# Kernel tuning notes

Measured on AMD Instinct MI355X. Metric: run time of the kernel, lower is better.

The kernel has to match this reference:

```python
import jax, jax.numpy as jnp
import numpy as np

B, T, C, H = 8, 2048, 1024, 64


def setup_inputs() -> dict:
    key = jax.random.key(0)
    kx, kq, kk, kv = jax.random.split(key, 4)
    sc = 1.0 / np.sqrt(C)
    return {
        "x": jax.random.normal(kx, (B, T, C), dtype=jnp.float32),
        "Wq": jax.random.normal(kq, (C, H), dtype=jnp.float32) * sc,
        "Wk": jax.random.normal(kk, (C, H), dtype=jnp.float32) * sc,
        "Wv": jax.random.normal(kv, (C, H), dtype=jnp.float32) * sc,
    }


def reference(x, Wq, Wk, Wv):
    # Projections: Linear(C, head_size, bias=False) == x @ W
    q = jnp.einsum("btc,ch->bth", x, Wq)
    k = jnp.einsum("btc,ch->bth", x, Wk)
    v = jnp.einsum("btc,ch->bth", x, Wv)
    head_size = q.shape[-1]
    scale = head_size ** -0.5
    # scores: [B, T, T]
    scores = jnp.einsum("bqh,bkh->bqk", q, k) * scale
    # causal mask (tril==0 -> -inf)
    causal = jnp.tril(jnp.ones((scores.shape[1], scores.shape[2]), dtype=bool))
    scores = jnp.where(causal, scores, -jnp.inf)
    w = jax.nn.softmax(scores, axis=-1)
    # dropout_rate=0.0 -> identity
    out = jnp.einsum("bqk,bkh->bqh", w, v)
    return out
```

## Files before the change

kernel.cpp:

```cpp
#include <hip/hip_runtime.h>
#include <hip/hip_bf16.h>
#include <cstdint>
#include <cstddef>

typedef short bf16x8 __attribute__((ext_vector_type(8)));
typedef float f32x4 __attribute__((ext_vector_type(4)));

#define BN 8
#define TN 2048
#define CN 1024
#define HN 64

__device__ __forceinline__ unsigned short f2bf(float f) {
    unsigned int u = __float_as_uint(f);
    u += 0x7fffu + ((u >> 16) & 1u);
    return (unsigned short)(u >> 16);
}

__device__ __forceinline__ int pk2(float lo, float hi) {
    float2 t; t.x = lo; t.y = hi;
    __hip_bfloat162 h = __float22bfloat162_rn(t);
    return *reinterpret_cast<int*>(&h);
}

__device__ __forceinline__ void gload_lds16(const unsigned short* gsrc, void* ldst) {
    __builtin_amdgcn_global_load_lds(
        (const __attribute__((address_space(1))) unsigned int*)gsrc,
        (__attribute__((address_space(3))) unsigned int*)ldst,
        16, 0, 0);
}

__global__ __launch_bounds__(256) void wconv_kernel(const float* __restrict__ Wq,
                                                    const float* __restrict__ Wk,
                                                    const float* __restrict__ Wv,
                                                    unsigned short* __restrict__ Wp) {
    int idx = blockIdx.x * 256 + threadIdx.x;
    int n = idx >> 10;
    int c = idx & 1023;
    int m = n >> 6;
    int h = n & 63;
    const float* W = (m == 0) ? Wq : ((m == 1) ? Wk : Wv);
    float v = W[c * 64 + h];
    if (m == 0) v *= 0.18033688011112042f;
    const int tile = n >> 4, lq = n & 15;
    const int kk = c >> 5, lg = (c >> 3) & 3, e = c & 7;
    Wp[(size_t)(((tile * 32 + kk) * 64 + lg * 16 + lq) * 8 + e)] = f2bf(v);
}

__global__ __launch_bounds__(256) void proj_kernel(const float* __restrict__ X,
                                                   const unsigned short* __restrict__ Wp,
                                                   unsigned short* __restrict__ Qs,
                                                   unsigned short* __restrict__ Kp,
                                                   unsigned short* __restrict__ Vp) {
    __shared__ short Xs[2][32 * 64];
    __shared__ short Wsh[2][6144];

    const int tid = threadIdx.x;
    const int w   = tid >> 6;
    const int l   = tid & 63;
    const int lq  = l & 15;
    const int lg  = l >> 4;
    const int wr   = w >> 1;
    const int nsub = w & 1;
    const int bid = blockIdx.x;
    const int mtile = bid & 511;
    const int nh    = bid >> 9;
    const int rowbase = mtile * 32;

    const int xrow = tid >> 3;
    const int xcol = (tid & 7) * 8;
    const float* xsrc = X + (size_t)(rowbase + xrow) * CN + xcol;
    const int xdst = xrow * 128 + ((xcol * 2) ^ ((xrow & 7) << 4));

    const unsigned short* wsrcc[3];
    int wdstc[3];
    #pragma unroll
    for (int i = 0; i < 3; ++i) {
        const int c = w * 3 + i;
        const int t = c >> 1, kkL = c & 1;
        wsrcc[i] = Wp + (size_t)((nh * 6 + t) * 32 + kkL) * 512 + l * 8;
        wdstc[i] = c * 1024;
    }

    const int arow = wr * 16 + lq;
    int aaddr[2];
    #pragma unroll
    for (int kkL = 0; kkL < 2; ++kkL)
        aaddr[kkL] = arow * 128 + (((kkL * 64 + lg * 16)) ^ ((arow & 7) << 4));
    int baddr[2][3];
    #pragma unroll
    for (int kkL = 0; kkL < 2; ++kkL)
        #pragma unroll
        for (int jj = 0; jj < 3; ++jj) {
            const int t = nsub * 3 + jj;
            baddr[kkL][jj] = ((t * 2 + kkL) * 512 + l * 8) * 2;
        }

    const f32x4 zero4 = {0.f, 0.f, 0.f, 0.f};
    f32x4 acc[3] = {zero4, zero4, zero4};

    {
        #pragma unroll
        for (int i = 0; i < 3; ++i)
            gload_lds16(wsrcc[i], (char*)Wsh[0] + wdstc[i]);
        float4 xa = *(const float4*)(xsrc);
        float4 xb = *(const float4*)(xsrc + 4);
        int4 xc;
        xc.x = pk2(xa.x, xa.y); xc.y = pk2(xa.z, xa.w);
        xc.z = pk2(xb.x, xb.y); xc.w = pk2(xb.z, xb.w);
        *(int4*)((char*)Xs[0] + xdst) = xc;
        __syncthreads();
    }

    for (int s = 0; s < 16; ++s) {
        const int cur = s & 1;
        const int nxt = cur ^ 1;
        const bool more = (s + 1) < 16;
        float4 xa, xb;
        if (more) {
            xa = *(const float4*)(xsrc + (s + 1) * 64);
            xb = *(const float4*)(xsrc + (s + 1) * 64 + 4);
            #pragma unroll
            for (int i = 0; i < 3; ++i)
                gload_lds16(wsrcc[i] + (s + 1) * 1024, (char*)Wsh[nxt] + wdstc[i]);
        }
        #pragma unroll
        for (int kkL = 0; kkL < 2; ++kkL) {
            bf16x8 a  = *(const bf16x8*)((char*)Xs[cur] + aaddr[kkL]);
            bf16x8 b0 = *(const bf16x8*)((char*)Wsh[cur] + baddr[kkL][0]);
            bf16x8 b1 = *(const bf16x8*)((char*)Wsh[cur] + baddr[kkL][1]);
            bf16x8 b2 = *(const bf16x8*)((char*)Wsh[cur] + baddr[kkL][2]);
            acc[0] = __builtin_amdgcn_mfma_f32_16x16x32_bf16(a, b0, acc[0], 0, 0, 0);
            acc[1] = __builtin_amdgcn_mfma_f32_16x16x32_bf16(a, b1, acc[1], 0, 0, 0);
            acc[2] = __builtin_amdgcn_mfma_f32_16x16x32_bf16(a, b2, acc[2], 0, 0, 0);
        }
        if (more) {
            int4 xc;
            xc.x = pk2(xa.x, xa.y); xc.y = pk2(xa.z, xa.w);
            xc.z = pk2(xb.x, xb.y); xc.w = pk2(xb.z, xb.w);
            *(int4*)((char*)Xs[nxt] + xdst) = xc;
        }
        __syncthreads();
    }

    #pragma unroll
    for (int jj = 0; jj < 3; ++jj) {
        const int col = nh * 96 + nsub * 48 + jj * 16 + lq;
        const int mtx = col >> 6;
        const int h   = col & 63;
        #pragma unroll
        for (int i = 0; i < 4; ++i) {
            const int g = rowbase + wr * 16 + 4 * lg + i;
            const unsigned short val = f2bf(acc[jj][i]);
            const int b = g >> 11, tloc = g & 2047;
            const int kt = tloc >> 5;
            if (mtx == 0) {
                Qs[(size_t)g * 64 + h] = val;
            } else if (mtx == 1) {
                const int fa = (tloc >> 4) & 1, lqk = tloc & 15;
                const int ks = h >> 5, lgk = (h >> 3) & 3, e = h & 7;
                Kp[(size_t)(b * 64 + kt) * 2048 + (fa * 2 + ks) * 512 +
                   (lgk * 16 + lqk) * 8 + e] = val;
            } else {
                const int tt = tloc & 31;
                const int lgv = (tt & 15) >> 2;
                const int e = (tt < 16) ? (tt & 3) : 4 + (tt & 3);
                const int nf = h >> 4, lqv = h & 15;
                Vp[(size_t)(b * 64 + kt) * 2048 + nf * 512 +
                   (lgv * 16 + lqv) * 8 + e] = val;
            }
        }
    }
}

__global__ __launch_bounds__(256) void attn_kernel(const unsigned short* __restrict__ Qs,
                                                   const unsigned short* __restrict__ Kp,
                                                   const unsigned short* __restrict__ Vp,
                                                   float* __restrict__ Out) {
    __shared__ float lm[4][16];
    __shared__ float ll[4][16];
    __shared__ float facc[4][1024];

    const int tid = threadIdx.x;
    const int w  = tid >> 6;
    const int l  = tid & 63;
    const int lq = l & 15;
    const int lg = l >> 4;
    const int bid = blockIdx.x;
    const int qt = 127 - (bid >> 3);
    const int b  = bid & 7;
    const int q0 = qt * 16;
    const int nt = (qt >> 1) + 1;

    const unsigned short* Qb = Qs + (size_t)b * TN * 64;
    const unsigned short* KVbase_k = Kp + (size_t)b * 64 * 2048 + (size_t)l * 8;
    const unsigned short* KVbase_v = Vp + (size_t)b * 64 * 2048 + (size_t)l * 8;

    const f32x4 zero4 = {0.f, 0.f, 0.f, 0.f};

    bf16x8 qa0 = *(const bf16x8*)(Qb + (size_t)(q0 + lq) * 64 + lg * 8);
    bf16x8 qa1 = *(const bf16x8*)(Qb + (size_t)(q0 + lq) * 64 + 32 + lg * 8);

    f32x4 acc[4] = {zero4, zero4, zero4, zero4};
    float mrow = -1e30f;
    float lrow = 0.f;

    bf16x8 Kc[4], Vc[4], Kn[4], Vn[4];
    int kt = w;
    if (kt < nt) {
        const size_t tb = (size_t)kt * 2048;
        #pragma unroll
        for (int i = 0; i < 4; ++i) {
            Kc[i] = *(const bf16x8*)(KVbase_k + tb + i * 512);
            Vc[i] = *(const bf16x8*)(KVbase_v + tb + i * 512);
        }
    }

    for (; kt < nt; kt += 4) {
        const int ktn = kt + 4;
        if (ktn < nt) {
            const size_t tb = (size_t)ktn * 2048;
            #pragma unroll
            for (int i = 0; i < 4; ++i) {
                Kn[i] = *(const bf16x8*)(KVbase_k + tb + i * 512);
                Vn[i] = *(const bf16x8*)(KVbase_v + tb + i * 512);
            }
        }

        const int key0 = kt * 32;
        f32x4 s[2];
        s[0] = __builtin_amdgcn_mfma_f32_16x16x32_bf16(Kc[0], qa0, zero4, 0, 0, 0);
        s[0] = __builtin_amdgcn_mfma_f32_16x16x32_bf16(Kc[1], qa1, s[0], 0, 0, 0);
        s[1] = __builtin_amdgcn_mfma_f32_16x16x32_bf16(Kc[2], qa0, zero4, 0, 0, 0);
        s[1] = __builtin_amdgcn_mfma_f32_16x16x32_bf16(Kc[3], qa1, s[1], 0, 0, 0);

        if (kt == nt - 1) {
            const int q = q0 + lq;
            #pragma unroll
            for (int fa = 0; fa < 2; ++fa)
                #pragma unroll
                for (int r = 0; r < 4; ++r) {
                    const int key = key0 + fa * 16 + 4 * lg + r;
                    if (key > q) s[fa][r] = -1e30f;
                }
        }

        float m1 = fmaxf(fmaxf(s[0][0], s[0][1]), s[0][2]);
        float m2 = fmaxf(fmaxf(s[0][3], s[1][0]), s[1][1]);
        float m3 = fmaxf(fmaxf(s[1][2], s[1][3]), m1);
        float tm = fmaxf(m2, m3);
        tm = fmaxf(tm, __shfl_xor(tm, 16));
        tm = fmaxf(tm, __shfl_xor(tm, 32));

        if (!__all(tm <= mrow + 8.0f)) {
            const float mnew = fmaxf(mrow, tm);
            const float cc = __builtin_amdgcn_exp2f(mrow - mnew);
            lrow *= cc;
            float cb[4];
            #pragma unroll
            for (int i = 0; i < 4; ++i) cb[i] = __shfl(cc, 4 * lg + i);
            #pragma unroll
            for (int nf = 0; nf < 4; ++nf)
                #pragma unroll
                for (int i = 0; i < 4; ++i) acc[nf][i] *= cb[i];
            mrow = mnew;
        }

        float p[2][4];
        float psum = 0.f;
        #pragma unroll
        for (int fa = 0; fa < 2; ++fa)
            #pragma unroll
            for (int r = 0; r < 4; ++r) {
                p[fa][r] = __builtin_amdgcn_exp2f(s[fa][r] - mrow);
                psum += p[fa][r];
            }
        psum += __shfl_xor(psum, 16);
        psum += __shfl_xor(psum, 32);
        lrow += psum;

        bf16x8 pa;
        pa[0] = (short)f2bf(p[0][0]); pa[1] = (short)f2bf(p[0][1]);
        pa[2] = (short)f2bf(p[0][2]); pa[3] = (short)f2bf(p[0][3]);
        pa[4] = (short)f2bf(p[1][0]); pa[5] = (short)f2bf(p[1][1]);
        pa[6] = (short)f2bf(p[1][2]); pa[7] = (short)f2bf(p[1][3]);

        acc[0] = __builtin_amdgcn_mfma_f32_16x16x32_bf16(pa, Vc[0], acc[0], 0, 0, 0);
        acc[1] = __builtin_amdgcn_mfma_f32_16x16x32_bf16(pa, Vc[1], acc[1], 0, 0, 0);
        acc[2] = __builtin_amdgcn_mfma_f32_16x16x32_bf16(pa, Vc[2], acc[2], 0, 0, 0);
        acc[3] = __builtin_amdgcn_mfma_f32_16x16x32_bf16(pa, Vc[3], acc[3], 0, 0, 0);

        #pragma unroll
        for (int i = 0; i < 4; ++i) { Kc[i] = Kn[i]; Vc[i] = Vn[i]; }
    }

    if (lg == 0) {
        lm[w][lq] = mrow;
        ll[w][lq] = lrow;
    }
    #pragma unroll
    for (int nf = 0; nf < 4; ++nf)
        #pragma unroll
        for (int i = 0; i < 4; ++i)
            facc[w][(4 * lg + i) * 64 + nf * 16 + lq] = acc[nf][i];

    __syncthreads();

    #pragma unroll
    for (int ii = 0; ii < 4; ++ii) {
        const int e = tid + ii * 256;
        const int q = e >> 6;
        const int h = e & 63;
        const float M = fmaxf(fmaxf(lm[0][q], lm[1][q]),
                              fmaxf(lm[2][q], lm[3][q]));
        float L = 0.f, O = 0.f;
        #pragma unroll
        for (int c = 0; c < 4; ++c) {
            const float wgt = __builtin_amdgcn_exp2f(lm[c][q] - M);
            L += wgt * ll[c][q];
            O += wgt * facc[c][q * 64 + h];
        }
        Out[((size_t)b * TN + q0 + q) * 64 + h] = O / L;
    }
}

extern "C" void kernel_launch(void* const* d_in, const int* in_sizes, int n_in,
                              void* d_out, int out_size, void* d_ws, size_t ws_size,
                              hipStream_t stream) {
    const float* X  = (const float*)d_in[0];
    const float* Wq = (const float*)d_in[1];
    const float* Wk = (const float*)d_in[2];
    const float* Wv = (const float*)d_in[3];
    float* Out = (float*)d_out;

    char* ws = (char*)d_ws;
    unsigned short* Wp = (unsigned short*)(ws);
    unsigned short* Qs = (unsigned short*)(ws + (512u << 10));
    unsigned short* Kp = Qs + (size_t)16384 * 64;
    unsigned short* Vp = Kp + (size_t)16384 * 64;

    hipLaunchKernelGGL(wconv_kernel, dim3(768), dim3(256), 0, stream, Wq, Wk, Wv, Wp);
    hipLaunchKernelGGL(proj_kernel,  dim3(1024), dim3(256), 0, stream, X, Wp, Qs, Kp, Vp);
    hipLaunchKernelGGL(attn_kernel,  dim3(1024), dim3(256), 0, stream, Qs, Kp, Vp, Out);
}
```

Before: 44.87 us.

## Use 4-stage LDS ring with async direct loads for X and W in projection

The projection kernel now loads fp32 X tiles straight into LDS through global_load_lds, alongside the W tiles, instead of going through registers with bf16 packing before the LDS store. A 4-slot ring buffer with prefetch distance 2 and explicit vmcnt waits and s_barriers replaces the double buffer. The aim is to hide global latency better and drop the register staging of X. In exchange, fp32 X takes twice the LDS space, and the bf16 conversion now happens after the LDS read on every compute step.

```diff
diff --git a/kernel.cpp b/kernel.cpp
--- a/kernel.cpp
+++ b/kernel.cpp
@@ -23,7 +23,7 @@
     return *reinterpret_cast<int*>(&h);
 }
 
-__device__ __forceinline__ void gload_lds16(const unsigned short* gsrc, void* ldst) {
+__device__ __forceinline__ void gload16(const void* gsrc, void* ldst) {
     __builtin_amdgcn_global_load_lds(
         (const __attribute__((address_space(1))) unsigned int*)gsrc,
         (__attribute__((address_space(3))) unsigned int*)ldst,
@@ -52,8 +52,7 @@
                                                    unsigned short* __restrict__ Qs,
                                                    unsigned short* __restrict__ Kp,
                                                    unsigned short* __restrict__ Vp) {
-    __shared__ short Xs[2][32 * 64];
-    __shared__ short Wsh[2][6144];
+    __shared__ __align__(16) char ring[4][20480];
 
     const int tid = threadIdx.x;
     const int w   = tid >> 6;
@@ -67,80 +66,89 @@
     const int nh    = bid >> 9;
     const int rowbase = mtile * 32;
 
-    const int xrow = tid >> 3;
-    const int xcol = (tid & 7) * 8;
-    const float* xsrc = X + (size_t)(rowbase + xrow) * CN + xcol;
-    const int xdst = xrow * 128 + ((xcol * 2) ^ ((xrow & 7) << 4));
-
-    const unsigned short* wsrcc[3];
-    int wdstc[3];
+    const unsigned short* wsrc[3];
+    int wdst[3];
     #pragma unroll
     for (int i = 0; i < 3; ++i) {
         const int c = w * 3 + i;
         const int t = c >> 1, kkL = c & 1;
-        wsrcc[i] = Wp + (size_t)((nh * 6 + t) * 32 + kkL) * 512 + l * 8;
-        wdstc[i] = c * 1024;
+        wsrc[i] = Wp + (size_t)((nh * 6 + t) * 32 + kkL) * 512 + l * 8;
+        wdst[i] = c * 1024;
+    }
+    const float* xg[2];
+    int xdst[2];
+    #pragma unroll
+    for (int i = 0; i < 2; ++i) {
+        const int c = 2 * w + i;
+        const int r = c * 4 + (l >> 4);
+        xg[i] = X + (size_t)(rowbase + r) * CN + 4 * ((l & 15) ^ (r & 7));
+        xdst[i] = 12288 + c * 1024;
     }
 
     const int arow = wr * 16 + lq;
-    int aaddr[2];
+    const int aswz = (arow & 7) << 4;
+    int axoff[2][2];
     #pragma unroll
     for (int kkL = 0; kkL < 2; ++kkL)
-        aaddr[kkL] = arow * 128 + (((kkL * 64 + lg * 16)) ^ ((arow & 7) << 4));
-    int baddr[2][3];
+        #pragma unroll
+        for (int h = 0; h < 2; ++h)
+            axoff[kkL][h] = 12288 + arow * 256 + ((kkL * 128 + lg * 32 + h * 16) ^ aswz);
+    int bwoff[2][3];
     #pragma unroll
     for (int kkL = 0; kkL < 2; ++kkL)
         #pragma unroll
         for (int jj = 0; jj < 3; ++jj) {
             const int t = nsub * 3 + jj;
-            baddr[kkL][jj] = ((t * 2 + kkL) * 512 + l * 8) * 2;
+            bwoff[kkL][jj] = (t * 2 + kkL) * 1024 + l * 16;
         }
 
     const f32x4 zero4 = {0.f, 0.f, 0.f, 0.f};
     f32x4 acc[3] = {zero4, zero4, zero4};
 
-    {
-        #pragma unroll
-        for (int i = 0; i < 3; ++i)
-            gload_lds16(wsrcc[i], (char*)Wsh[0] + wdstc[i]);
-        float4 xa = *(const float4*)(xsrc);
-        float4 xb = *(const float4*)(xsrc + 4);
-        int4 xc;
-        xc.x = pk2(xa.x, xa.y); xc.y = pk2(xa.z, xa.w);
-        xc.z = pk2(xb.x, xb.y); xc.w = pk2(xb.z, xb.w);
-        *(int4*)((char*)Xs[0] + xdst) = xc;
-        __syncthreads();
+    #pragma unroll
+    for (int t = 0; t < 2; ++t) {
+        char* base = ring[t];
+        gload16(wsrc[0] + t * 1024, base + wdst[0]);
+        gload16(wsrc[1] + t * 1024, base + wdst[1]);
+        gload16(wsrc[2] + t * 1024, base + wdst[2]);
+        gload16(xg[0] + t * 64, base + xdst[0]);
+        gload16(xg[1] + t * 64, base + xdst[1]);
     }
 
     for (int s = 0; s < 16; ++s) {
-        const int cur = s & 1;
-        const int nxt = cur ^ 1;
-        const bool more = (s + 1) < 16;
-        float4 xa, xb;
-        if (more) {
-            xa = *(const float4*)(xsrc + (s + 1) * 64);
-            xb = *(const float4*)(xsrc + (s + 1) * 64 + 4);
-            #pragma unroll
-            for (int i = 0; i < 3; ++i)
-                gload_lds16(wsrcc[i] + (s + 1) * 1024, (char*)Wsh[nxt] + wdstc[i]);
-        }
-        #pragma unroll
-        for (int kkL = 0; kkL < 2; ++kkL) {
-            bf16x8 a  = *(const bf16x8*)((char*)Xs[cur] + aaddr[kkL]);
-            bf16x8 b0 = *(const bf16x8*)((char*)Wsh[cur] + baddr[kkL][0]);
-            bf16x8 b1 = *(const bf16x8*)((char*)Wsh[cur] + baddr[kkL][1]);
-            bf16x8 b2 = *(const bf16x8*)((char*)Wsh[cur] + baddr[kkL][2]);
-            acc[0] = __builtin_amdgcn_mfma_f32_16x16x32_bf16(a, b0, acc[0], 0, 0, 0);
-            acc[1] = __builtin_amdgcn_mfma_f32_16x16x32_bf16(a, b1, acc[1], 0, 0, 0);
-            acc[2] = __builtin_amdgcn_mfma_f32_16x16x32_bf16(a, b2, acc[2], 0, 0, 0);
-        }
-        if (more) {
-            int4 xc;
-            xc.x = pk2(xa.x, xa.y); xc.y = pk2(xa.z, xa.w);
-            xc.z = pk2(xb.x, xb.y); xc.w = pk2(xb.z, xb.w);
-            *(int4*)((char*)Xs[nxt] + xdst) = xc;
-        }
-        __syncthreads();
+        if (s <= 13) {
+            char* base = ring[(s + 2) & 3];
+            gload16(wsrc[0] + (s + 2) * 1024, base + wdst[0]);
+            gload16(wsrc[1] + (s + 2) * 1024, base + wdst[1]);
+            gload16(wsrc[2] + (s + 2) * 1024, base + wdst[2]);
+            gload16(xg[0] + (s + 2) * 64, base + xdst[0]);
+            gload16(xg[1] + (s + 2) * 64, base + xdst[1]);
+            asm volatile("s_waitcnt vmcnt(10)" ::: "memory");
+        } else if (s == 14) {
+            asm volatile("s_waitcnt vmcnt(5)" ::: "memory");
+        } else {
+            asm volatile("s_waitcnt vmcnt(0)" ::: "memory");
+        }
+        asm volatile("s_barrier" ::: "memory");
+        __builtin_amdgcn_sched_barrier(0);
+        {
+            const char* base = ring[s & 3];
+            #pragma unroll
+            for (int kkL = 0; kkL < 2; ++kkL) {
+                float4 xa = *(const float4*)(base + axoff[kkL][0]);
+                float4 xb = *(const float4*)(base + axoff[kkL][1]);
+                union { bf16x8 v; int u[4]; } ua;
+                ua.u[0] = pk2(xa.x, xa.y); ua.u[1] = pk2(xa.z, xa.w);
+                ua.u[2] = pk2(xb.x, xb.y); ua.u[3] = pk2(xb.z, xb.w);
+                #pragma unroll
+                for (int jj = 0; jj < 3; ++jj) {
+                    bf16x8 b = *(const bf16x8*)(base + bwoff[kkL][jj]);
+                    acc[jj] = __builtin_amdgcn_mfma_f32_16x16x32_bf16(ua.v, b, acc[jj], 0, 0, 0);
+                }
+            }
+        }
+        __builtin_amdgcn_sched_barrier(0);
+        asm volatile("s_barrier" ::: "memory");
     }
 
     #pragma unroll
```

Result: slower. 54.77 us (+22.1%).
